# Kernel tuning notes

Hardware: AMD Instinct MI355X
Metric: run time of the kernel (lower is better)

The kernel has to match this reference:

```python
import jax, jax.numpy as jnp
import numpy as np
import math

DIM = 1024; B = 4; S = 2048; R = 3; K = 256; MAXR = 256; H = 8; HD = DIM // H
THRESH = 0.5; EPS = 1e-5

def _gelu(x):
    return jax.nn.gelu(x, approximate=False)

def _ln(x, g, b):
    m = jnp.mean(x, axis=-1, keepdims=True)
    v = jnp.var(x, axis=-1, keepdims=True)
    return (x - m) * jax.lax.rsqrt(v + EPS) * g + b

def setup_inputs() -> dict:
    key = jax.random.key(0)
    ks = jax.random.split(key, 24)
    sd = 1.0 / math.sqrt(DIM)
    sd2 = 1.0 / math.sqrt(2 * DIM)
    return {
        'x': jax.random.normal(ks[0], (B, S, DIM), jnp.float32),
        'retrieved': jax.random.normal(ks[1], (R, B, K, DIM), jnp.float32),
        # per-retriever query generator MLPs: Linear->GELU->Linear
        'qg_w1': jax.random.normal(ks[2], (R, DIM, DIM), jnp.float32) * sd,
        'qg_b1': jnp.zeros((R, DIM), jnp.float32),
        'qg_w2': jax.random.normal(ks[3], (R, DIM, DIM), jnp.float32) * sd,
        'qg_b2': jnp.zeros((R, DIM), jnp.float32),
        # per-retriever pooler: LayerNorm -> Linear
        'pln_g': jnp.ones((R, DIM), jnp.float32),
        'pln_b': jnp.zeros((R, DIM), jnp.float32),
        'pool_w': jax.random.normal(ks[4], (R, DIM, DIM), jnp.float32) * sd,
        'pool_b': jnp.zeros((R, DIM), jnp.float32),
        # relevance scorer: Linear(2d,d/2)->GELU->Linear(d/2,1)->Sigmoid
        'rel_w1': jax.random.normal(ks[5], (2 * DIM, DIM // 2), jnp.float32) * sd2,
        'rel_b1': jnp.zeros((DIM // 2,), jnp.float32),
        'rel_w2': jax.random.normal(ks[6], (DIM // 2, 1), jnp.float32) * (1.0 / math.sqrt(DIM // 2)),
        'rel_b2': jnp.zeros((1,), jnp.float32),
        # fusion MultiheadAttention: stacked q/k/v in-proj + out-proj
        'in_w': jax.random.normal(ks[7], (3, DIM, DIM), jnp.float32) * sd,
        'in_b': jnp.zeros((3, DIM), jnp.float32),
        'out_w': jax.random.normal(ks[8], (DIM, DIM), jnp.float32) * sd,
        'out_b': jnp.zeros((DIM,), jnp.float32),
        # fusion LayerNorm
        'fln_g': jnp.ones((DIM,), jnp.float32),
        'fln_b': jnp.zeros((DIM,), jnp.float32),
    }

def reference(x, retrieved, qg_w1, qg_b1, qg_w2, qg_b2, pln_g, pln_b, pool_w, pool_b,
              rel_w1, rel_b1, rel_w2, rel_b2, in_w, in_b, out_w, out_b, fln_g, fln_b):
    # ---- query generation: per-retriever MLP + self-attn pooling ----
    qf = _gelu(jnp.einsum('bsd,rde->rbse', x, qg_w1) + qg_b1[:, None, None, :])
    qf = jnp.einsum('rbsd,rde->rbse', qf, qg_w2) + qg_b2[:, None, None, :]  # [R,B,S,D]
    attn = jax.nn.softmax(jnp.einsum('rbsd,rbtd->rbst', qf, qf) / math.sqrt(DIM), axis=-1)
    pooled = jnp.einsum('rbst,rbtd->rbsd', attn, qf).mean(axis=2)  # [R,B,D]
    pooled = _ln(pooled, pln_g[:, None, :], pln_b[:, None, :])
    queries = jnp.einsum('rbd,rde->rbe', pooled, pool_w) + pool_b[:, None, :]  # [R,B,D]
    # ---- relevance scoring of retrieved tokens against queries ----
    q_exp = jnp.broadcast_to(queries[:, :, None, :], (R, B, K, DIM))
    pairs = jnp.concatenate([retrieved, q_exp], axis=-1)  # [R,B,K,2D]
    h = _gelu(pairs @ rel_w1 + rel_b1)
    rel = jax.nn.sigmoid((h @ rel_w2 + rel_b2)[..., 0])  # [R,B,K]
    # ---- threshold mask + per-batch top-k across all retrievers ----
    cand_tok = jnp.transpose(retrieved, (1, 0, 2, 3)).reshape(B, R * K, DIM)
    cand_rel = jnp.transpose(rel, (1, 0, 2)).reshape(B, R * K)
    valid = cand_rel >= THRESH
    masked_rel = jnp.where(valid, cand_rel, -jnp.inf)
    _, top_idx = jax.lax.top_k(masked_rel, MAXR)  # [B,MAXR]
    sel_tok = jnp.take_along_axis(cand_tok, top_idx[..., None], axis=1)  # [B,MAXR,D]
    key_valid = jnp.take_along_axis(valid, top_idx, axis=1)  # [B,MAXR]
    any_valid = jnp.any(key_valid, axis=-1)  # [B]
    # ---- fusion: cross-attention x -> selected tokens, residual + LN ----
    q = (x @ in_w[0] + in_b[0]).reshape(B, S, H, HD)
    k = (sel_tok @ in_w[1] + in_b[1]).reshape(B, MAXR, H, HD)
    v = (sel_tok @ in_w[2] + in_b[2]).reshape(B, MAXR, H, HD)
    scores = jnp.einsum('bshd,bthd->bhst', q, k) / math.sqrt(HD)
    scores = jnp.where(key_valid[:, None, None, :], scores, -1e9)
    a = jax.nn.softmax(scores, axis=-1)
    fused = jnp.einsum('bhst,bthd->bshd', a, v).reshape(B, S, DIM) @ out_w + out_b
    enhanced = _ln(x + fused, fln_g, fln_b)
    return jnp.where(any_valid[:, None, None], enhanced, x)
```

## Files before the change

kernel.cpp:

```cpp
#include <hip/hip_runtime.h>
#include <math.h>


typedef unsigned short u16;
typedef unsigned int   u32;
typedef __attribute__((ext_vector_type(8))) short short8;
typedef __attribute__((ext_vector_type(4))) float f32x4;
typedef __attribute__((ext_vector_type(4))) u16  u16x4;

__device__ __forceinline__ float b2f(u16 u){ union{float f;u32 i;} x; x.i=((u32)u)<<16; return x.f; }
__device__ __forceinline__ u16 f2b(float f){ union{float f;u32 i;} x; x.f=f; u32 r=x.i+0x7fffu+((x.i>>16)&1u); return (u16)(r>>16); }
__device__ __forceinline__ float gelu_f(float v){ return 0.5f*v*(1.f+erff(v*0.70710678118654752f)); }

__device__ __forceinline__ void load_lds16(const u16* g, u16* l){
  __builtin_amdgcn_global_load_lds((const __attribute__((address_space(1))) u32*)g,
                                   (__attribute__((address_space(3))) u32*)l, 16, 0, 0);
}

__device__ __forceinline__ float waveRedSum(float v){
  #pragma unroll
  for (int o=32;o>0;o>>=1) v += __shfl_xor(v,o);
  return v;
}
__device__ __forceinline__ float waveRedMax(float v){
  #pragma unroll
  for (int o=32;o>0;o>>=1) v = fmaxf(v, __shfl_xor(v,o));
  return v;
}
__device__ float blockRedSum(float v){
  __shared__ float tmp[17];
  const int lane = threadIdx.x&63, wv = threadIdx.x>>6, nw = blockDim.x>>6;
  v = waveRedSum(v);
  __syncthreads();
  if (lane==0) tmp[wv]=v;
  __syncthreads();
  if (threadIdx.x==0){ float s=tmp[0]; for(int i=1;i<nw;i++) s+=tmp[i]; tmp[16]=s; }
  __syncthreads();
  return tmp[16];
}
__device__ float blockRedMax(float v){
  __shared__ float tmp[17];
  const int lane = threadIdx.x&63, wv = threadIdx.x>>6, nw = blockDim.x>>6;
  v = waveRedMax(v);
  __syncthreads();
  if (lane==0) tmp[wv]=v;
  __syncthreads();
  if (threadIdx.x==0){ float s=tmp[0]; for(int i=1;i<nw;i++) s=fmaxf(s,tmp[i]); tmp[16]=s; }
  __syncthreads();
  return tmp[16];
}

enum { EPI_NONE=0, EPI_BIAS=1, EPI_SCALE=3, EPI_VT=5 };

template<int EPI>
__global__ __launch_bounds__(256,2)
void gemm_nt(const u16* __restrict__ Ag, long long lda, long long sA1, long long sA2,
             const u16* __restrict__ Bg, long long ldb, long long sB1, long long sB2,
             u16* __restrict__ Cg, long long ldc, long long sC1, long long sC2,
             const float* __restrict__ bias, long long sBias,
             float scale, int K, int H)
{
  __shared__ u16 As[128*32];
  __shared__ u16 Bs[128*32];
  const int z  = blockIdx.z;
  const int zb = z / H, zh = z - zb*H;
  const u16* A = Ag + zb*sA1 + zh*sA2;
  const u16* B = Bg + zb*sB1 + zh*sB2;
  const int m0 = blockIdx.y*128, n0 = blockIdx.x*128;
  const int t  = threadIdx.x;
  const int lane = t & 63, wv = t >> 6;
  const int wm = (wv>>1)*64, wn = (wv&1)*64;

  const u16* ga0 = A + (long long)(m0 + (t>>2))*lda + (t&3)*8;
  const u16* ga1 = ga0 + 64*lda;
  const u16* gb0 = B + (long long)(n0 + (t>>2))*ldb + (t&3)*8;
  const u16* gb1 = gb0 + 64*ldb;
  u16* lA0 = As + t*8;  u16* lA1 = As + 2048 + t*8;
  u16* lB0 = Bs + t*8;  u16* lB1 = Bs + 2048 + t*8;

  f32x4 acc[4][4];
  #pragma unroll
  for (int i=0;i<4;i++)
    #pragma unroll
    for (int j=0;j<4;j++) acc[i][j] = (f32x4){0.f,0.f,0.f,0.f};

  const short8* arp = (const short8*)(As + (wm + (lane&15))*32 + ((lane>>4)*8));
  const short8* brp = (const short8*)(Bs + (wn + (lane&15))*32 + ((lane>>4)*8));

  for (int kk = 0; kk < K; kk += 32) {
    load_lds16(ga0, lA0); load_lds16(ga1, lA1);
    load_lds16(gb0, lB0); load_lds16(gb1, lB1);
    ga0 += 32; ga1 += 32; gb0 += 32; gb1 += 32;
    __syncthreads();
    short8 af[4], bfr[4];
    #pragma unroll
    for (int i=0;i<4;i++) af[i]  = arp[i*64];
    #pragma unroll
    for (int j=0;j<4;j++) bfr[j] = brp[j*64];
    #pragma unroll
    for (int i=0;i<4;i++)
      #pragma unroll
      for (int j=0;j<4;j++)
        acc[i][j] = __builtin_amdgcn_mfma_f32_16x16x32_bf16(af[i], bfr[j], acc[i][j], 0, 0, 0);
    __syncthreads();
  }

  u16* C = Cg + zb*sC1 + zh*sC2;
  const float* bz = bias + zb*sBias;
  const int rb0 = m0 + wm + ((lane>>4)<<2);
  const int cb0 = n0 + wn + (lane&15);
  #pragma unroll
  for (int j=0;j<4;j++){
    const int cn = cb0 + j*16;
    float bv = 0.f;
    if constexpr (EPI==EPI_BIAS || EPI==EPI_VT) bv = bz[cn];
    #pragma unroll
    for (int i=0;i<4;i++){
      #pragma unroll
      for (int p=0;p<4;p++){
        const int row = rb0 + i*16 + p;
        float v = acc[i][j][p];
        if constexpr (EPI==EPI_SCALE) v *= scale;
        if constexpr (EPI==EPI_BIAS)  v += bv;
        if constexpr (EPI==EPI_VT) {
          v += bv;
          const int bb = row>>8, tt = row&255, hh = cn>>7, dd = cn&127;
          C[((long long)((bb*8+hh)*128+dd)<<8) + tt] = f2b(v);
        } else {
          C[(long long)row*ldc + cn] = f2b(v);
        }
      }
    }
  }
}

enum { SP_GELU_SPLIT=0, SP_BIAS_SPLIT=1, SP_SCALE_F32=2, SP_QBG_F32=3 };

template<int EPI>
__global__ __launch_bounds__(256,2)
void gemm_nt_split(const u16* __restrict__ Ah_, const u16* __restrict__ Al_, long long lda, long long sAz,
                   const u16* __restrict__ Bh_, const u16* __restrict__ Bl_, long long ldb, long long sBz,
                   void* __restrict__ C0, void* __restrict__ C1, long long ldc, long long sCz,
                   const float* __restrict__ bias, float scale, int K)
{
  __shared__ u16 AsH[128*32];
  __shared__ u16 AsL[128*32];
  __shared__ u16 BsH[128*32];
  __shared__ u16 BsL[128*32];
  const int z = blockIdx.z;
  const int m0 = blockIdx.y*128, n0 = blockIdx.x*128;
  const int t  = threadIdx.x;
  const int lane = t & 63, wv = t >> 6;
  const int wm = (wv>>1)*64, wn = (wv&1)*64;

  const long long arow = (long long)z*sAz + (long long)(m0 + (t>>2))*lda + (t&3)*8;
  const long long brow = (long long)z*sBz + (long long)(n0 + (t>>2))*ldb + (t&3)*8;
  const u16* gah0 = Ah_ + arow;  const u16* gah1 = gah0 + 64*lda;
  const u16* gal0 = Al_ + arow;  const u16* gal1 = gal0 + 64*lda;
  const u16* gbh0 = Bh_ + brow;  const u16* gbh1 = gbh0 + 64*ldb;
  const u16* gbl0 = Bl_ + brow;  const u16* gbl1 = gbl0 + 64*ldb;
  u16* lAh0 = AsH + t*8;  u16* lAh1 = AsH + 2048 + t*8;
  u16* lAl0 = AsL + t*8;  u16* lAl1 = AsL + 2048 + t*8;
  u16* lBh0 = BsH + t*8;  u16* lBh1 = BsH + 2048 + t*8;
  u16* lBl0 = BsL + t*8;  u16* lBl1 = BsL + 2048 + t*8;

  f32x4 acc[4][4];
  #pragma unroll
  for (int i=0;i<4;i++)
    #pragma unroll
    for (int j=0;j<4;j++) acc[i][j] = (f32x4){0.f,0.f,0.f,0.f};

  const int foff = (lane&15)*32 + ((lane>>4)*8);
  const short8* arh = (const short8*)(AsH + wm*32 + foff);
  const short8* arl = (const short8*)(AsL + wm*32 + foff);
  const short8* brh = (const short8*)(BsH + wn*32 + foff);
  const short8* brl = (const short8*)(BsL + wn*32 + foff);

  for (int kk = 0; kk < K; kk += 32) {
    load_lds16(gah0, lAh0); load_lds16(gah1, lAh1);
    load_lds16(gal0, lAl0); load_lds16(gal1, lAl1);
    load_lds16(gbh0, lBh0); load_lds16(gbh1, lBh1);
    load_lds16(gbl0, lBl0); load_lds16(gbl1, lBl1);
    gah0 += 32; gah1 += 32; gal0 += 32; gal1 += 32;
    gbh0 += 32; gbh1 += 32; gbl0 += 32; gbl1 += 32;
    __syncthreads();
    short8 fah[4], fal[4], fbh[4], fbl[4];
    #pragma unroll
    for (int i=0;i<4;i++){ fah[i]=arh[i*64]; fal[i]=arl[i*64]; }
    #pragma unroll
    for (int j=0;j<4;j++){ fbh[j]=brh[j*64]; fbl[j]=brl[j*64]; }
    #pragma unroll
    for (int i=0;i<4;i++)
      #pragma unroll
      for (int j=0;j<4;j++){
        acc[i][j] = __builtin_amdgcn_mfma_f32_16x16x32_bf16(fal[i], fbh[j], acc[i][j], 0, 0, 0);
        acc[i][j] = __builtin_amdgcn_mfma_f32_16x16x32_bf16(fah[i], fbl[j], acc[i][j], 0, 0, 0);
        acc[i][j] = __builtin_amdgcn_mfma_f32_16x16x32_bf16(fah[i], fbh[j], acc[i][j], 0, 0, 0);
      }
    __syncthreads();
  }

  const int rb0 = m0 + wm + ((lane>>4)<<2);
  const int cb0 = n0 + wn + (lane&15);
  #pragma unroll
  for (int j=0;j<4;j++){
    const int cn = cb0 + j*16;
    float bv = 0.f;
    if constexpr (EPI==SP_GELU_SPLIT || EPI==SP_BIAS_SPLIT) bv = bias[cn];
    #pragma unroll
    for (int i=0;i<4;i++){
      #pragma unroll
      for (int p=0;p<4;p++){
        const int row = rb0 + i*16 + p;
        float v = acc[i][j][p];
        const long long o = (long long)z*sCz + (long long)row*ldc + cn;
        if constexpr (EPI==SP_GELU_SPLIT || EPI==SP_BIAS_SPLIT){
          v += bv;
          if constexpr (EPI==SP_GELU_SPLIT) v = gelu_f(v);
          const u16 h = f2b(v);
          ((u16*)C0)[o] = h;
          ((u16*)C1)[o] = f2b(v - b2f(h));
        }
        if constexpr (EPI==SP_SCALE_F32) ((float*)C0)[o] = v*scale;
        if constexpr (EPI==SP_QBG_F32)   ((float*)C0)[o] = gelu_f(v + bias[(row>>8)*512 + cn]);
      }
    }
  }
}

__global__ void transpose_w(const float* __restrict__ in, u16* __restrict__ out, int rows, int cols){
  __shared__ float tl[32][33];
  const long long zo = (long long)blockIdx.z*rows*cols;
  const int c0 = blockIdx.x*32, r0 = blockIdx.y*32;
  const int tx = threadIdx.x, ty = threadIdx.y;
  #pragma unroll
  for (int yy=ty; yy<32; yy+=8) tl[yy][tx] = in[zo + (long long)(r0+yy)*cols + (c0+tx)];
  __syncthreads();
  #pragma unroll
  for (int yy=ty; yy<32; yy+=8) out[zo + (long long)(c0+yy)*rows + (r0+tx)] = f2b(tl[tx][yy]);
}

__global__ void split_transpose_w(const float* __restrict__ in, u16* __restrict__ outH,
                                  u16* __restrict__ outL, int rows, int cols){
  __shared__ float tl[32][33];
  const long long zo = (long long)blockIdx.z*rows*cols;
  const int c0 = blockIdx.x*32, r0 = blockIdx.y*32;
  const int tx = threadIdx.x, ty = threadIdx.y;
  #pragma unroll
  for (int yy=ty; yy<32; yy+=8) tl[yy][tx] = in[zo + (long long)(r0+yy)*cols + (c0+tx)];
  __syncthreads();
  #pragma unroll
  for (int yy=ty; yy<32; yy+=8){
    const float v = tl[tx][yy];
    const u16 h = f2b(v);
    const long long o = zo + (long long)(c0+yy)*rows + (r0+tx);
    outH[o] = h;
    outL[o] = f2b(v - b2f(h));
  }
}

__global__ void split_f32_k(const float* __restrict__ in, u16* __restrict__ oh,
                            u16* __restrict__ ol, int n4){
  const int i = blockIdx.x*256 + threadIdx.x;
  if (i < n4){
    const float4 v = ((const float4*)in)[i];
    u16x4 hh, ll;
    hh.x=f2b(v.x); ll.x=f2b(v.x-b2f(hh.x));
    hh.y=f2b(v.y); ll.y=f2b(v.y-b2f(hh.y));
    hh.z=f2b(v.z); ll.z=f2b(v.z-b2f(hh.z));
    hh.w=f2b(v.w); ll.w=f2b(v.w-b2f(hh.w));
    ((u16x4*)oh)[i] = hh;
    ((u16x4*)ol)[i] = ll;
  }
}

__global__ void zero_f32(float* __restrict__ p, int n){
  const int i = blockIdx.x*256 + threadIdx.x;
  if (i < n) p[i] = 0.f;
}

__global__ void init_queries(const float* __restrict__ pb, float* __restrict__ q){
  const int i = blockIdx.x*256 + threadIdx.x;
  if (i < 12288) q[i] = pb[(i>>12)*1024 + (i&1023)];
}
__global__ void init_qpart(const float* __restrict__ rb1, float* __restrict__ qp){
  const int i = blockIdx.x*256 + threadIdx.x;
  if (i < 6144) qp[i] = rb1[i&511];
}

__global__ void ws_report(float* __restrict__ out, int n4, float val){
  const int i = blockIdx.x*256 + threadIdx.x;
  if (i < n4){
    float4 z; z.x = (i==0)? val : 0.f; z.y=0.f; z.z=0.f; z.w=0.f;
    ((float4*)out)[i] = z;
  }
}

__global__ void row_stats_f32(const float* __restrict__ S, float* __restrict__ mOut,
                              float* __restrict__ dOut){
  const int row = blockIdx.x;
  const float4* p = (const float4*)(S + (long long)row*2048);
  const int tid = threadIdx.x;
  const float4 a = p[2*tid], b = p[2*tid+1];
  float v[8] = {a.x,a.y,a.z,a.w,b.x,b.y,b.z,b.w};
  float mx = v[0];
  #pragma unroll
  for (int k=1;k<8;k++) mx = fmaxf(mx, v[k]);
  mx = blockRedMax(mx);
  float s = 0.f;
  #pragma unroll
  for (int k=0;k<8;k++) s += expf(v[k]-mx);
  s = blockRedSum(s);
  if (tid==0){ mOut[row]=mx; dOut[row]=s; }
}

__global__ void col_mean_f32(const float* __restrict__ S, const float* __restrict__ m,
                             const float* __restrict__ den, float* __restrict__ w){
  const int tc = blockIdx.x*256 + threadIdx.x;
  const int s0 = blockIdx.y*64;
  const float* p = S + (long long)s0*2048 + tc;
  float acc = 0.f;
  for (int s=0;s<64;s++)
    acc += expf(p[(long long)s<<11] - m[s0+s]) * (1.0f/den[s0+s]);
  atomicAdd(&w[tc], acc * (1.f/2048.f));
}

__global__ __launch_bounds__(256)
void pooled_par(const u16* __restrict__ qfh, const u16* __restrict__ qfl,
                const float* __restrict__ w, float* __restrict__ pooled){
  const int b = blockIdx.x, tt0 = blockIdx.y*128;
  const int t = threadIdx.x;
  __shared__ float wsh[128];
  if (t < 128) wsh[t] = w[b*2048 + tt0 + t];
  __syncthreads();
  const long long base = (long long)b*2097152 + (long long)tt0*1024;
  const u16* ph = qfh + base;
  const u16* pl = qfl + base;
  float acc[4] = {0.f,0.f,0.f,0.f};
  for (int s=0; s<128; s++){
    const float wt = wsh[s];
    const long long o = (long long)s*1024;
    #pragma unroll
    for (int k=0;k<4;k++){
      const int dd = t + k*256;
      acc[k] += wt*(b2f(ph[o+dd]) + b2f(pl[o+dd]));
    }
  }
  #pragma unroll
  for (int k=0;k<4;k++) atomicAdd(&pooled[b*1024 + t + k*256], acc[k]);
}

__global__ __launch_bounds__(1024)
void pool_ln(const float* __restrict__ pooled, const float* __restrict__ pg,
             const float* __restrict__ pb, float* __restrict__ plbuf){
  const int z = blockIdx.x, r = z>>2, d = threadIdx.x;
  const float v = pooled[z*1024+d];
  const float mean = blockRedSum(v) * (1.f/1024.f);
  const float df = v - mean;
  const float var = blockRedSum(df*df) * (1.f/1024.f);
  plbuf[z*1024+d] = df*rsqrtf(var+1e-5f)*pg[r*1024+d] + pb[r*1024+d];
}

__global__ __launch_bounds__(256)
void query_accum(const float* __restrict__ plbuf, const float* __restrict__ pw,
                 float* __restrict__ queries){
  const int z = blockIdx.x, r = z>>2, k0 = blockIdx.y*32;
  const int t = threadIdx.x;
  __shared__ float pls[32];
  if (t < 32) pls[t] = plbuf[z*1024 + k0 + t];
  __syncthreads();
  const float* wp = pw + (long long)r*1048576 + (long long)k0*1024;
  float acc[4] = {0.f,0.f,0.f,0.f};
  for (int s=0;s<32;s++){
    const float wv = pls[s];
    #pragma unroll
    for (int c=0;c<4;c++) acc[c] += wv*wp[s*1024 + t + c*256];
  }
  #pragma unroll
  for (int c=0;c<4;c++) atomicAdd(&queries[z*1024 + t + c*256], acc[c]);
}

__global__ __launch_bounds__(256)
void qpart_accum(const float* __restrict__ queries, const float* __restrict__ rw1,
                 float* __restrict__ qpart){
  const int z = blockIdx.x, k0 = blockIdx.y*64;
  const int t = threadIdx.x;
  __shared__ float qs[64];
  if (t < 64) qs[t] = queries[z*1024 + k0 + t];
  __syncthreads();
  const float* wp = rw1 + 1024*512 + (long long)k0*512;
  float acc[2] = {0.f,0.f};
  for (int s=0;s<64;s++){
    const float wv = qs[s];
    #pragma unroll
    for (int c=0;c<2;c++) acc[c] += wv*wp[s*512 + t + c*256];
  }
  #pragma unroll
  for (int c=0;c<2;c++) atomicAdd(&qpart[z*512 + t + c*256], acc[c]);
}

__global__ void rel_score_f32(const float* __restrict__ h, const float* __restrict__ w2,
                              const float* __restrict__ b2p, float* __restrict__ relv){
  const int row = blockIdx.x*4 + (threadIdx.x>>6);
  const int lane = threadIdx.x & 63;
  const float* p = h + (long long)row*512;
  float a = 0.f;
  #pragma unroll
  for (int k=0;k<8;k++){ const int idx = lane + k*64; a += p[idx]*w2[idx]; }
  a = waveRedSum(a);
  if (lane==0){
    const float lg = a + b2p[0];
    relv[row] = 1.f/(1.f+expf(-lg));
  }
}

__global__ __launch_bounds__(768)
void select_topk(const float* __restrict__ relv, int* __restrict__ selidx,
                 int* __restrict__ neff, int* __restrict__ anyv){
  const int b = blockIdx.x, c = threadIdx.x;
  __shared__ float rv[768];
  __shared__ int cnt;
  rv[c] = relv[(((c>>8)*4)+b)*256 + (c&255)];
  if (c==0) cnt = 0;
  __syncthreads();
  const float mine = rv[c];
  const bool valid = (mine >= 0.5f);
  int rank = 0;
  for (int j=0;j<768;j++){
    const float vj = rv[j];
    if (vj >= 0.5f && (vj > mine || (vj == mine && j < c))) rank++;
  }
  if (valid && rank < 256){
    const int s = atomicAdd(&cnt, 1);
    selidx[b*256 + s] = c;
  }
  __syncthreads();
  if (c==0){ neff[b] = cnt; anyv[b] = (cnt>0) ? 1 : 0; }
}

__global__ void gather_sel(const u16* __restrict__ rb16, const int* __restrict__ selidx,
                           const int* __restrict__ neff, u16* __restrict__ seltok){
  const int slot = blockIdx.x, b = blockIdx.y, tid = threadIdx.x;
  uint2 val; val.x=0u; val.y=0u;
  if (slot < neff[b]){
    const int c = selidx[b*256+slot];
    const uint2* src = (const uint2*)(rb16 + (long long)(((c>>8)*4+b)*256 + (c&255))*1024);
    val = src[tid];
  }
  ((uint2*)(seltok + (long long)(b*256+slot)*1024))[tid] = val;
}

__global__ void attn_softmax(u16* __restrict__ S, const int* __restrict__ neff){
  const int ri = blockIdx.x*4 + (threadIdx.x>>6);
  const int lane = threadIdx.x & 63;
  const int b = ri >> 14;
  const int ne = neff[b];
  u16* p = S + (long long)ri*256 + lane*4;
  if (ne == 0){ uint2 zz; zz.x=0u; zz.y=0u; *(uint2*)p = zz; return; }
  uint2 raw = *(const uint2*)p;
  u16 uu[4] = {(u16)(raw.x&0xffffu),(u16)(raw.x>>16),(u16)(raw.y&0xffffu),(u16)(raw.y>>16)};
  float xs[4];
  #pragma unroll
  for (int q2=0;q2<4;q2++){ const int tt = lane*4+q2; xs[q2] = (tt<ne)? b2f(uu[q2]) : -1e30f; }
  float mx = fmaxf(fmaxf(xs[0],xs[1]),fmaxf(xs[2],xs[3]));
  mx = waveRedMax(mx);
  float e[4]; float sm=0.f;
  #pragma unroll
  for (int q2=0;q2<4;q2++){ e[q2] = (lane*4+q2<ne)? expf(xs[q2]-mx) : 0.f; sm += e[q2]; }
  sm = waveRedSum(sm);
  const float inv = 1.f/sm;
  #pragma unroll
  for (int q2=0;q2<4;q2++) uu[q2] = f2b(e[q2]*inv);
  raw.x = (u32)uu[0] | ((u32)uu[1]<<16);
  raw.y = (u32)uu[2] | ((u32)uu[3]<<16);
  *(uint2*)p = raw;
}

__global__ void final_ln(const float* __restrict__ x, const u16* __restrict__ fused,
                         const float* __restrict__ g, const float* __restrict__ bb,
                         const int* __restrict__ anyv, float* __restrict__ out){
  const int row = blockIdx.x; const int b = row>>11; const int tid = threadIdx.x;
  const float4 xv = ((const float4*)(x + (long long)row*1024))[tid];
  const uint2 fv = ((const uint2*)(fused + (long long)row*1024))[tid];
  const float e0 = xv.x + b2f((u16)(fv.x&0xffffu));
  const float e1 = xv.y + b2f((u16)(fv.x>>16));
  const float e2 = xv.z + b2f((u16)(fv.y&0xffffu));
  const float e3 = xv.w + b2f((u16)(fv.y>>16));
  const float mean = blockRedSum(e0+e1+e2+e3) * (1.f/1024.f);
  const float d0=e0-mean, d1=e1-mean, d2=e2-mean, d3=e3-mean;
  const float var = blockRedSum(d0*d0+d1*d1+d2*d2+d3*d3) * (1.f/1024.f);
  const float inv = rsqrtf(var + 1e-5f);
  const float4 gv = ((const float4*)g)[tid];
  const float4 bv = ((const float4*)bb)[tid];
  float4 o;
  if (anyv[b]){
    o.x = d0*inv*gv.x + bv.x; o.y = d1*inv*gv.y + bv.y;
    o.z = d2*inv*gv.z + bv.z; o.w = d3*inv*gv.w + bv.w;
  } else o = xv;
  ((float4*)(out + (long long)row*1024))[tid] = o;
}

extern "C" void kernel_launch(void* const* d_in, const int* in_sizes, int n_in,
                              void* d_out, int out_size, void* d_ws, size_t ws_size,
                              hipStream_t stream) {
  (void)in_sizes; (void)n_in;
  const float* x      = (const float*)d_in[0];
  const float* retr   = (const float*)d_in[1];
  const float* qg_w1  = (const float*)d_in[2];
  const float* qg_b1  = (const float*)d_in[3];
  const float* qg_w2  = (const float*)d_in[4];
  const float* qg_b2  = (const float*)d_in[5];
  const float* pln_g  = (const float*)d_in[6];
  const float* pln_b  = (const float*)d_in[7];
  const float* pool_w = (const float*)d_in[8];
  const float* pool_b = (const float*)d_in[9];
  const float* rel_w1 = (const float*)d_in[10];
  const float* rel_b1 = (const float*)d_in[11];
  const float* rel_w2 = (const float*)d_in[12];
  const float* rel_b2 = (const float*)d_in[13];
  const float* in_w   = (const float*)d_in[14];
  const float* in_b   = (const float*)d_in[15];
  const float* out_w  = (const float*)d_in[16];
  const float* out_b  = (const float*)d_in[17];
  const float* fln_g  = (const float*)d_in[18];
  const float* fln_b  = (const float*)d_in[19];
  float* out = (float*)d_out;
  char* ws = (char*)d_ws;

  const size_t MB = 1u<<20;
  const size_t REQUIRED = 131*MB;
  if (ws_size < REQUIRED){
    ws_report<<<(out_size/4 + 255)/256, 256, 0, stream>>>(out, out_size/4, (float)(ws_size>>20));
    return;
  }

  u16* qg1Th = (u16*)(ws + 0*MB);
  u16* qg1Tl = (u16*)(ws + 6*MB);
  u16* qg2Th = (u16*)(ws + 12*MB);
  u16* qg2Tl = (u16*)(ws + 18*MB);
  u16* xh    = (u16*)(ws + 24*MB);
  u16* xl    = (u16*)(ws + 40*MB);
  u16* qfh   = (u16*)(ws + 56*MB);
  u16* qfl   = (u16*)(ws + 72*MB);
  u16* t1h   = (u16*)(ws + 88*MB);
  u16* t1l   = (u16*)(ws + 104*MB);
  float* scoresA = (float*)(ws + 88*MB);
  float* scoresB = (float*)(ws + 104*MB);
  u16* rh    = (u16*)(ws + 0*MB);
  u16* rl    = (u16*)(ws + 6*MB);
  u16* relTh = (u16*)(ws + 12*MB);
  u16* relTl = (u16*)(ws + 13*MB);
  u16* seltok= (u16*)(ws + 14*MB);
  u16* kbuf  = (u16*)(ws + 16*MB);
  u16* VT    = (u16*)(ws + 18*MB);
  float* hbuf= (float*)(ws + 88*MB);
  u16* inT   = (u16*)(ws + 40*MB);
  u16* outT  = (u16*)(ws + 46*MB);
  u16* qbuf  = (u16*)(ws + 56*MB);
  u16* fused = (u16*)(ws + 72*MB);
  u16* Sattn = (u16*)(ws + 88*MB);
  u16* attnout=(u16*)(ws + 0*MB);
  char* SM = ws + 120*MB;
  float* wbuf    = (float*)(SM);
  float* pooledB = (float*)(SM + 98304);
  float* plbuf   = (float*)(SM + 147456);
  float* queries = (float*)(SM + 196608);
  float* qpart   = (float*)(SM + 245760);
  float* relv    = (float*)(SM + 270336);
  int*   selidx  = (int*)(SM + 282624);
  int*   neff    = (int*)(SM + 286720);
  int*   anyv    = (int*)(SM + 286784);
  float* mrow0   = (float*)(SM + 286848);
  float* drow0   = (float*)(SM + 295040);
  float* mrow1   = (float*)(SM + 303232);
  float* drow1   = (float*)(SM + 311424);

  dim3 b256(256);
  dim3 tb(32,8);
  const long long SCZ = (long long)(16*MB)/4;

  split_transpose_w<<<dim3(32,32,3), tb, 0, stream>>>(qg_w1, qg1Th, qg1Tl, 1024, 1024);
  split_transpose_w<<<dim3(32,32,3), tb, 0, stream>>>(qg_w2, qg2Th, qg2Tl, 1024, 1024);
  split_f32_k<<<8192, b256, 0, stream>>>(x, xh, xl, 2097152);
  zero_f32<<<144, b256, 0, stream>>>(wbuf, 36864);

  for (int r = 0; r < 3; r++){
    const long long wo = (long long)r*1048576;
    gemm_nt_split<SP_GELU_SPLIT><<<dim3(8,64,1), b256, 0, stream>>>(
        xh, xl, 1024, 0,  qg1Th+wo, qg1Tl+wo, 1024, 0,
        t1h, t1l, 1024, 0,  qg_b1+r*1024, 1.f, 1024);
    gemm_nt_split<SP_BIAS_SPLIT><<<dim3(8,64,1), b256, 0, stream>>>(
        t1h, t1l, 1024, 0,  qg2Th+wo, qg2Tl+wo, 1024, 0,
        qfh, qfl, 1024, 0,  qg_b2+r*1024, 1.f, 1024);
    for (int p2 = 0; p2 < 2; p2++){
      const long long qo = (long long)(p2*2)*2097152;
      gemm_nt_split<SP_SCALE_F32><<<dim3(16,16,2), b256, 0, stream>>>(
          qfh+qo, qfl+qo, 1024, 2097152,  qfh+qo, qfl+qo, 1024, 2097152,
          scoresA, nullptr, 2048, SCZ,  nullptr, 0.03125f, 1024);
      row_stats_f32<<<2048, b256, 0, stream>>>(scoresA, mrow0, drow0);
      row_stats_f32<<<2048, b256, 0, stream>>>(scoresB, mrow1, drow1);
      col_mean_f32<<<dim3(8,32), b256, 0, stream>>>(scoresA, mrow0, drow0, wbuf + (r*4+p2*2  )*2048);
      col_mean_f32<<<dim3(8,32), b256, 0, stream>>>(scoresB, mrow1, drow1, wbuf + (r*4+p2*2+1)*2048);
    }
    pooled_par<<<dim3(4,16), b256, 0, stream>>>(qfh, qfl, wbuf + r*8192, pooledB + r*4096);
  }
  pool_ln<<<12, 1024, 0, stream>>>(pooledB, pln_g, pln_b, plbuf);
  init_queries<<<48, b256, 0, stream>>>(pool_b, queries);
  query_accum<<<dim3(12,32), b256, 0, stream>>>(plbuf, pool_w, queries);

  split_f32_k<<<3072, b256, 0, stream>>>(retr, rh, rl, 786432);
  split_transpose_w<<<dim3(16,32,1), tb, 0, stream>>>(rel_w1, relTh, relTl, 1024, 512);
  init_qpart<<<24, b256, 0, stream>>>(rel_b1, qpart);
  qpart_accum<<<dim3(12,16), b256, 0, stream>>>(queries, rel_w1, qpart);
  gemm_nt_split<SP_QBG_F32><<<dim3(4,24,1), b256, 0, stream>>>(
      rh, rl, 1024, 0,  relTh, relTl, 1024, 0,  hbuf, nullptr, 512, 0,  qpart, 1.f, 1024);
  rel_score_f32<<<768, b256, 0, stream>>>(hbuf, rel_w2, rel_b2, relv);

  select_topk<<<4, 768, 0, stream>>>(relv, selidx, neff, anyv);
  gather_sel<<<dim3(256,4), b256, 0, stream>>>(rh, selidx, neff, seltok);

  transpose_w<<<dim3(32,32,3), tb, 0, stream>>>(in_w,  inT,  1024, 1024);
  transpose_w<<<dim3(32,32,1), tb, 0, stream>>>(out_w, outT, 1024, 1024);
  gemm_nt<EPI_BIAS><<<dim3(8,64,1), b256, 0, stream>>>(
      xh,1024,0,0,  inT,1024,0,0,  qbuf,1024,0,0,  in_b,0, 1.f, 1024, 1);
  gemm_nt<EPI_BIAS><<<dim3(8,8,1), b256, 0, stream>>>(
      seltok,1024,0,0,  inT+1048576,1024,0,0,  kbuf,1024,0,0,  in_b+1024,0, 1.f, 1024, 1);
  gemm_nt<EPI_VT><<<dim3(8,8,1), b256, 0, stream>>>(
      seltok,1024,0,0,  inT+2097152,1024,0,0,  VT,0,0,0,  in_b+2048,0, 1.f, 1024, 1);
  gemm_nt<EPI_SCALE><<<dim3(2,16,32), b256, 0, stream>>>(
      qbuf,1024,2097152,128,  kbuf,1024,262144,128,  Sattn,256,4194304,524288,
      (const float*)nullptr,0, 0.08838834764831845f, 128, 8);
  attn_softmax<<<16384, b256, 0, stream>>>(Sattn, neff);
  gemm_nt<EPI_NONE><<<dim3(1,16,32), b256, 0, stream>>>(
      Sattn,256,4194304,524288,  VT,256,262144,32768,  attnout,1024,2097152,128,
      (const float*)nullptr,0, 1.f, 256, 8);
  gemm_nt<EPI_BIAS><<<dim3(8,64,1), b256, 0, stream>>>(
      attnout,1024,0,0,  outT,1024,0,0,  fused,1024,0,0,  out_b,0, 1.f, 1024, 1);
  final_ln<<<8192, b256, 0, stream>>>(x, fused, fln_g, fln_b, anyv, out);
}
```

Baseline: 1.535 ms.

## Double-buffer LDS tiles in GEMM kernels to overlap global loads with MFMA

Both the plain and the split-bf16 GEMM kernels now keep two LDS tile buffers. The next K-slice is issued via global_load_lds while MFMAs run on the current slice, and a single vmcnt wait plus barrier closes each iteration instead of two syncthreads. The goal is to hide global memory latency behind matrix math. In exchange, LDS use per block doubles (64KB for the split kernel), which may limit the two-blocks-per-CU occupancy target.

```diff
diff --git a/kernel.cpp b/kernel.cpp
--- a/kernel.cpp
+++ b/kernel.cpp
@@ -60,8 +60,8 @@
              const float* __restrict__ bias, long long sBias,
              float scale, int K, int H)
 {
-  __shared__ u16 As[128*32];
-  __shared__ u16 Bs[128*32];
+  __shared__ u16 As[2*4096];
+  __shared__ u16 Bs[2*4096];
   const int z  = blockIdx.z;
   const int zb = z / H, zh = z - zb*H;
   const u16* A = Ag + zb*sA1 + zh*sA2;
@@ -87,23 +87,34 @@
   const short8* arp = (const short8*)(As + (wm + (lane&15))*32 + ((lane>>4)*8));
   const short8* brp = (const short8*)(Bs + (wn + (lane&15))*32 + ((lane>>4)*8));
 
-  for (int kk = 0; kk < K; kk += 32) {
-    load_lds16(ga0, lA0); load_lds16(ga1, lA1);
-    load_lds16(gb0, lB0); load_lds16(gb1, lB1);
-    ga0 += 32; ga1 += 32; gb0 += 32; gb1 += 32;
-    __syncthreads();
+  #define STAGE_NT(bo) do{ \
+    load_lds16(ga0, lA0+(bo)); load_lds16(ga1, lA1+(bo)); \
+    load_lds16(gb0, lB0+(bo)); load_lds16(gb1, lB1+(bo)); \
+    ga0 += 32; ga1 += 32; gb0 += 32; gb1 += 32; }while(0)
+
+  const int nk = K >> 5;
+  STAGE_NT(0);
+  asm volatile("s_waitcnt vmcnt(0)" ::: "memory");
+  __builtin_amdgcn_s_barrier();
+  int cur = 0;
+  for (int kk = 0; kk < nk; ++kk) {
+    if (kk+1 < nk) STAGE_NT((cur^1)*4096);
+    const int boS = cur*512;
     short8 af[4], bfr[4];
     #pragma unroll
-    for (int i=0;i<4;i++) af[i]  = arp[i*64];
-    #pragma unroll
-    for (int j=0;j<4;j++) bfr[j] = brp[j*64];
+    for (int i=0;i<4;i++) af[i]  = arp[boS + i*64];
+    #pragma unroll
+    for (int j=0;j<4;j++) bfr[j] = brp[boS + j*64];
     #pragma unroll
     for (int i=0;i<4;i++)
       #pragma unroll
       for (int j=0;j<4;j++)
         acc[i][j] = __builtin_amdgcn_mfma_f32_16x16x32_bf16(af[i], bfr[j], acc[i][j], 0, 0, 0);
-    __syncthreads();
-  }
+    asm volatile("s_waitcnt vmcnt(0)" ::: "memory");
+    __builtin_amdgcn_s_barrier();
+    cur ^= 1;
+  }
+  #undef STAGE_NT
 
   u16* C = Cg + zb*sC1 + zh*sC2;
   const float* bz = bias + zb*sBias;
@@ -143,10 +154,10 @@
                    void* __restrict__ C0, void* __restrict__ C1, long long ldc, long long sCz,
                    const float* __restrict__ bias, float scale, int K)
 {
-  __shared__ u16 AsH[128*32];
-  __shared__ u16 AsL[128*32];
-  __shared__ u16 BsH[128*32];
-  __shared__ u16 BsL[128*32];
+  __shared__ u16 AsH[2*4096];
+  __shared__ u16 AsL[2*4096];
+  __shared__ u16 BsH[2*4096];
+  __shared__ u16 BsL[2*4096];
   const int z = blockIdx.z;
   const int m0 = blockIdx.y*128, n0 = blockIdx.x*128;
   const int t  = threadIdx.x;
@@ -176,19 +187,27 @@
   const short8* brh = (const short8*)(BsH + wn*32 + foff);
   const short8* brl = (const short8*)(BsL + wn*32 + foff);
 
-  for (int kk = 0; kk < K; kk += 32) {
-    load_lds16(gah0, lAh0); load_lds16(gah1, lAh1);
-    load_lds16(gal0, lAl0); load_lds16(gal1, lAl1);
-    load_lds16(gbh0, lBh0); load_lds16(gbh1, lBh1);
-    load_lds16(gbl0, lBl0); load_lds16(gbl1, lBl1);
-    gah0 += 32; gah1 += 32; gal0 += 32; gal1 += 32;
-    gbh0 += 32; gbh1 += 32; gbl0 += 32; gbl1 += 32;
-    __syncthreads();
+  #define STAGE_SP(bo) do{ \
+    load_lds16(gah0, lAh0+(bo)); load_lds16(gah1, lAh1+(bo)); \
+    load_lds16(gal0, lAl0+(bo)); load_lds16(gal1, lAl1+(bo)); \
+    load_lds16(gbh0, lBh0+(bo)); load_lds16(gbh1, lBh1+(bo)); \
+    load_lds16(gbl0, lBl0+(bo)); load_lds16(gbl1, lBl1+(bo)); \
+    gah0 += 32; gah1 += 32; gal0 += 32; gal1 += 32; \
+    gbh0 += 32; gbh1 += 32; gbl0 += 32; gbl1 += 32; }while(0)
+
+  const int nk = K >> 5;
+  STAGE_SP(0);
+  asm volatile("s_waitcnt vmcnt(0)" ::: "memory");
+  __builtin_amdgcn_s_barrier();
+  int cur = 0;
+  for (int kk = 0; kk < nk; ++kk) {
+    if (kk+1 < nk) STAGE_SP((cur^1)*4096);
+    const int boS = cur*512;
     short8 fah[4], fal[4], fbh[4], fbl[4];
     #pragma unroll
-    for (int i=0;i<4;i++){ fah[i]=arh[i*64]; fal[i]=arl[i*64]; }
-    #pragma unroll
-    for (int j=0;j<4;j++){ fbh[j]=brh[j*64]; fbl[j]=brl[j*64]; }
+    for (int i=0;i<4;i++){ fah[i]=arh[boS+i*64]; fal[i]=arl[boS+i*64]; }
+    #pragma unroll
+    for (int j=0;j<4;j++){ fbh[j]=brh[boS+j*64]; fbl[j]=brl[boS+j*64]; }
     #pragma unroll
     for (int i=0;i<4;i++)
       #pragma unroll
@@ -197,8 +216,11 @@
         acc[i][j] = __builtin_amdgcn_mfma_f32_16x16x32_bf16(fah[i], fbl[j], acc[i][j], 0, 0, 0);
         acc[i][j] = __builtin_amdgcn_mfma_f32_16x16x32_bf16(fah[i], fbh[j], acc[i][j], 0, 0, 0);
       }
-    __syncthreads();
-  }
+    asm volatile("s_waitcnt vmcnt(0)" ::: "memory");
+    __builtin_amdgcn_s_barrier();
+    cur ^= 1;
+  }
+  #undef STAGE_SP
 
   const int rb0 = m0 + wm + ((lane>>4)<<2);
   const int cb0 = n0 + wn + (lane&15);
```

Result: faster. 1.415 ms (-7.9%).
